# Kernel optimization log

Measured on AMD Instinct MI355X. Metric: run time of the kernel, lower is better.

The kernel has to match this reference:

```python
import jax, jax.numpy as jnp
import numpy as np

NEG_INF = -1e10


def setup_inputs() -> dict:
    key = jax.random.key(0)
    ks = jax.random.split(key, 9)
    B, S, H, E = 64, 4096, 512, 512
    hidden = jax.random.normal(ks[0], (B, H), dtype=jnp.float32)
    encoder_outputs = jax.random.normal(ks[1], (B, S, E), dtype=jnp.float32)
    mask = jax.random.randint(ks[2], (B, S), 0, 2, dtype=jnp.int32)
    s = 1.0 / np.sqrt(H)
    Wq = jax.random.uniform(ks[3], (H, H), jnp.float32, -s, s)
    bq = jax.random.uniform(ks[4], (H,), jnp.float32, -s, s)
    se = 1.0 / np.sqrt(E)
    Wk = jax.random.uniform(ks[5], (E, H), jnp.float32, -se, se)
    bk = jax.random.uniform(ks[6], (H,), jnp.float32, -se, se)
    Wv = jax.random.uniform(ks[7], (H, 1), jnp.float32, -s, s)
    bv = jax.random.uniform(ks[8], (1,), jnp.float32, -s, s)
    return {"hidden": hidden, "encoder_outputs": encoder_outputs, "mask": mask,
            "Wq": Wq, "bq": bq, "Wk": Wk, "bk": bk, "Wv": Wv, "bv": bv}


def reference(hidden, encoder_outputs, mask, Wq, bq, Wk, bk, Wv, bv):
    # query projection: (B, H) -> broadcast over src_len
    q = hidden @ Wq + bq                       # (B, H)
    k = jnp.einsum('bse,eh->bsh', encoder_outputs, Wk) + bk  # (B, S, H)
    energy = jnp.tanh(q[:, None, :] + k)       # (B, S, H)
    scores = jnp.einsum('bsh,h->bs', energy, Wv[:, 0]) + bv[0]  # (B, S)
    scores = jnp.where(mask == 0, NEG_INF, scores)
    attn = jax.nn.softmax(scores, axis=1)      # (B, S)
    context = jnp.einsum('bs,bse->be', attn, encoder_outputs)   # (B, E)
    return context, attn
```

## Files before the change

kernel.cpp:

```cpp
#include <hip/hip_runtime.h>
#include <hip/hip_bf16.h>

#define B_ 64
#define S_ 4096
#define H_ 512
#define E_ 512
#define NEG_INF_ -1e10f

typedef __attribute__((ext_vector_type(8))) short short8;
typedef __attribute__((ext_vector_type(16))) float f32x16;

static __device__ __forceinline__ unsigned short f2bf(float f) {
    union { float f; unsigned u; } v; v.f = f;
    unsigned x = v.u;
    x += 0x7FFFu + ((x >> 16) & 1u);
    return (unsigned short)(x >> 16);
}

static __device__ __forceinline__ unsigned pk2(float lo, float hi) {
    float2 f; f.x = lo; f.y = hi;
    union { __hip_bfloat162 h; unsigned u; } c;
    c.h = __float22bfloat162_rn(f);
    return c.u;
}

static __device__ __forceinline__ void gload_lds16(const void* g, void* l) {
    __builtin_amdgcn_global_load_lds(
        (const __attribute__((address_space(1))) void*)g,
        (__attribute__((address_space(3))) void*)l, 16, 0, 0);
}

#define VMCNT12 do { asm volatile("s_waitcnt vmcnt(12)" ::: "memory"); __builtin_amdgcn_sched_barrier(0); } while (0)
#define VMCNT6  do { asm volatile("s_waitcnt vmcnt(6)"  ::: "memory"); __builtin_amdgcn_sched_barrier(0); } while (0)
#define VMCNT0  do { asm volatile("s_waitcnt vmcnt(0)"  ::: "memory"); __builtin_amdgcn_sched_barrier(0); } while (0)
#define LGKM0   do { asm volatile("s_waitcnt lgkmcnt(0)" ::: "memory"); __builtin_amdgcn_sched_barrier(0); } while (0)

__global__ void prep_wkt(const float* __restrict__ wk, unsigned short* __restrict__ wkt) {
    int idx = blockIdx.x * 256 + threadIdx.x;
    int h = idx >> 9, e = idx & 511;
    wkt[idx] = f2bf(wk[e * H_ + h]);
}

__global__ void prep_qb(const float* __restrict__ hidden, const float* __restrict__ wq,
                        const float* __restrict__ bq, const float* __restrict__ bk,
                        float* __restrict__ qb) {
    __shared__ float hid[H_];
    int b = blockIdx.x, t = threadIdx.x;
    hid[t]       = hidden[b * H_ + t];
    hid[t + 256] = hidden[b * H_ + t + 256];
    __syncthreads();
    for (int hh = t; hh < H_; hh += 256) {
        float s = 0.f;
        for (int e = 0; e < H_; ++e) s += hid[e] * wq[e * H_ + hh];
        qb[b * H_ + hh] = s + bq[hh] + bk[hh];
    }
}

__global__ __launch_bounds__(256, 3) void scores_kernel(
    const float* __restrict__ enc, const unsigned short* __restrict__ wkt,
    const float* __restrict__ qb, const float* __restrict__ wv,
    float* __restrict__ part)
{
    __shared__ char lds[49152];

    int id = blockIdx.x;
    int xcd = id & 7, qq = id >> 3;
    int logical = xcd * 1024 + qq;
    int b  = logical >> 7;
    int r  = logical & 127;
    int st = r >> 2, nt = r & 3;
    int s0 = st * 128;

    const int tid  = threadIdx.x;
    const int lane = tid & 63;
    const int wave = tid >> 6;
    const int wr   = wave >> 1;
    const int wc   = wave & 1;
    const int l31  = lane & 31;
    const int g    = lane >> 5;

    const float* encb = enc + ((size_t)b * S_ + s0) * E_;

    auto loadA = [&](int kc, float4 (&rg)[4]) {
#pragma unroll
        for (int j = 0; j < 2; ++j) {
            int sid = tid * 2 + j;
            int row = sid >> 2, ksl = sid & 3;
            const float* p = encb + (size_t)row * 512 + kc * 32 + ksl * 8;
            rg[j * 2 + 0] = *(const float4*)p;
            rg[j * 2 + 1] = *(const float4*)(p + 4);
        }
    };
    auto writeA = [&](char* buf, const float4 (&rg)[4]) {
#pragma unroll
        for (int j = 0; j < 2; ++j) {
            int sid = tid * 2 + j;
            int row = sid >> 2, ksl = sid & 3;
            int srow = row & 31;
            int sst  = ((row >> 5) * 4 + ksl) ^ (srow & 15);
            union { short8 s; unsigned u[4]; } u;
            u.u[0] = pk2(rg[j * 2].x, rg[j * 2].y);
            u.u[1] = pk2(rg[j * 2].z, rg[j * 2].w);
            u.u[2] = pk2(rg[j * 2 + 1].x, rg[j * 2 + 1].y);
            u.u[3] = pk2(rg[j * 2 + 1].z, rg[j * 2 + 1].w);
            *(short8*)(buf + srow * 256 + sst * 16) = u.s;
        }
    };
    auto stageB = [&](int kc, char* buf) {
#pragma unroll
        for (int p = 0; p < 2; ++p) {
            int gi0 = p * 256 + wave * 64;
            char* db = buf + gi0 * 16;
            int gi = gi0 + lane;
            int sn = gi >> 4, ss = gi & 15;
            int sl = ss ^ (sn & 15);
            int n  = (sl >> 2) * 32 + sn;
            const unsigned short* gp = wkt + (size_t)(nt * 128 + n) * 512 + kc * 32 + (sl & 3) * 8;
            gload_lds16(gp, db);
        }
    };

    f32x16 acc[2][2];
#pragma unroll
    for (int mr = 0; mr < 2; ++mr)
#pragma unroll
        for (int nf = 0; nf < 2; ++nf)
#pragma unroll
            for (int e = 0; e < 16; ++e) acc[mr][nf][e] = 0.f;

    float4 ra[4], rb[4], rc[4];

    stageB(0, lds + 16384);              loadA(0, ra);
    stageB(1, lds + 16384 + 8192);       loadA(1, rb);
    stageB(2, lds + 16384 + 16384);      loadA(2, rc);

    auto iter = [&](int kc, float4 (&rg)[4]) {
        if (kc <= 13) { VMCNT12; } else if (kc == 14) { VMCNT6; } else { VMCNT0; }
        char* Ab = lds + (kc & 1) * 8192;
        writeA(Ab, rg);
        LGKM0;
        __builtin_amdgcn_s_barrier();
        __builtin_amdgcn_sched_barrier(0);
        if (kc < 13) {
            stageB(kc + 3, lds + 16384 + ((kc + 3) & 3) * 8192);
            loadA(kc + 3, rg);
        }
        const char* Bb = lds + 16384 + (kc & 3) * 8192;
#pragma unroll
        for (int ks = 0; ks < 2; ++ks) {
            short8 af[2], bf[2];
#pragma unroll
            for (int mr = 0; mr < 2; ++mr) {
                int sl = (wr * 2 + mr) * 4 + ks * 2 + g;
                af[mr] = *(const short8*)(Ab + l31 * 256 + ((sl ^ (l31 & 15)) << 4));
            }
#pragma unroll
            for (int nf = 0; nf < 2; ++nf) {
                int sl = (wc * 2 + nf) * 4 + ks * 2 + g;
                bf[nf] = *(const short8*)(Bb + l31 * 256 + ((sl ^ (l31 & 15)) << 4));
            }
            acc[0][0] = __builtin_amdgcn_mfma_f32_32x32x16_bf16(af[0], bf[0], acc[0][0], 0, 0, 0);
            acc[0][1] = __builtin_amdgcn_mfma_f32_32x32x16_bf16(af[0], bf[1], acc[0][1], 0, 0, 0);
            acc[1][0] = __builtin_amdgcn_mfma_f32_32x32x16_bf16(af[1], bf[0], acc[1][0], 0, 0, 0);
            acc[1][1] = __builtin_amdgcn_mfma_f32_32x32x16_bf16(af[1], bf[1], acc[1][1], 0, 0, 0);
        }
    };

    for (int t3 = 0; t3 < 5; ++t3) {
        iter(t3 * 3,     ra);
        iter(t3 * 3 + 1, rb);
        iter(t3 * 3 + 2, rc);
    }
    iter(15, ra);

    float p[2][16];
#pragma unroll
    for (int nf = 0; nf < 2; ++nf) {
        int col = nt * 128 + wc * 64 + nf * 32 + l31;
        float qv  = qb[b * H_ + col];
        float wvv = wv[col];
#pragma unroll
        for (int mr = 0; mr < 2; ++mr)
#pragma unroll
            for (int e = 0; e < 16; ++e) {
                float x  = qv + acc[mr][nf][e];
                float ex = __expf(2.f * x);
                float th = 1.f - 2.f / (ex + 1.f);
                float v  = wvv * th;
                p[mr][e] = nf ? (p[mr][e] + v) : v;
            }
    }

    __syncthreads();
    float* ps = (float*)lds;
#pragma unroll
    for (int mr = 0; mr < 2; ++mr)
#pragma unroll
        for (int e = 0; e < 16; ++e) {
            int row = mr * 32 + (e & 3) + 8 * (e >> 2) + 4 * g;
            ps[(wave * 64 + row) * 36 + l31] = p[mr][e];
        }
    __syncthreads();
    float rsum = 0.f;
    {
        const float* myrow = ps + (size_t)(wave * 64 + lane) * 36;
#pragma unroll
        for (int j = 0; j < 8; ++j) {
            float4 v = *(const float4*)(myrow + j * 4);
            rsum += (v.x + v.y) + (v.z + v.w);
        }
    }
    float* pf = (float*)(lds + 37888);
    pf[wave * 64 + lane] = rsum;
    __syncthreads();
    if (tid < 128) {
        int wr2 = tid >> 6, rr = tid & 63;
        float v = pf[(wr2 * 2 + 0) * 64 + rr] + pf[(wr2 * 2 + 1) * 64 + rr];
        int s = s0 + wr2 * 64 + rr;
        part[((size_t)b * S_ + s) * 4 + nt] = v;
    }
}

__global__ void softmax_kernel(const float* __restrict__ part, const int* __restrict__ mask,
                               const float* __restrict__ bvp, float* __restrict__ attn) {
    __shared__ float red[8];
    int b = blockIdx.x, tid = threadIdx.x;
    int wid = tid >> 6, lane = tid & 63;
    float bv0 = bvp[0];
    float vals[8];
    float mx = -3.4e38f;
#pragma unroll
    for (int i = 0; i < 8; ++i) {
        int s = i * 512 + tid;
        float4 v = *(const float4*)(part + ((size_t)b * S_ + s) * 4);
        float sc = (v.x + v.y) + (v.z + v.w) + bv0;
        sc = mask[(size_t)b * S_ + s] ? sc : NEG_INF_;
        vals[i] = sc;
        mx = fmaxf(mx, sc);
    }
#pragma unroll
    for (int off = 1; off < 64; off <<= 1) mx = fmaxf(mx, __shfl_xor(mx, off));
    if (lane == 0) red[wid] = mx;
    __syncthreads();
    mx = red[0];
#pragma unroll
    for (int w = 1; w < 8; ++w) mx = fmaxf(mx, red[w]);
    __syncthreads();
    float sum = 0.f;
#pragma unroll
    for (int i = 0; i < 8; ++i) { vals[i] = __expf(vals[i] - mx); sum += vals[i]; }
#pragma unroll
    for (int off = 1; off < 64; off <<= 1) sum += __shfl_xor(sum, off);
    if (lane == 0) red[wid] = sum;
    __syncthreads();
    sum = red[0] + red[1] + red[2] + red[3] + red[4] + red[5] + red[6] + red[7];
    float inv = 1.f / sum;
#pragma unroll
    for (int i = 0; i < 8; ++i) attn[(size_t)b * S_ + i * 512 + tid] = vals[i] * inv;
}

__global__ void ctx_partial(const float* __restrict__ attn, const float* __restrict__ enc,
                            float* __restrict__ part) {
    __shared__ float a[256];
    int c = blockIdx.x, b = blockIdx.y, t = threadIdx.x;
    a[t] = attn[(size_t)b * S_ + c * 256 + t];
    __syncthreads();
    const float* ep = enc + (size_t)b * S_ * E_ + (size_t)c * 256 * E_ + t * 2;
    float x = 0.f, y = 0.f;
#pragma unroll 4
    for (int s = 0; s < 256; ++s) {
        float2 v = *(const float2*)(ep + (size_t)s * E_);
        x += a[s] * v.x;
        y += a[s] * v.y;
    }
    float* o = part + ((size_t)c * B_ + b) * E_ + t * 2;
    o[0] = x; o[1] = y;
}

__global__ void ctx_reduce(const float* __restrict__ part, float* __restrict__ ctx) {
    int idx = blockIdx.x * 256 + threadIdx.x;
    float s = 0.f;
#pragma unroll
    for (int c = 0; c < 16; ++c) s += part[(size_t)c * (B_ * E_) + idx];
    ctx[idx] = s;
}

extern "C" void kernel_launch(void* const* d_in, const int* in_sizes, int n_in,
                              void* d_out, int out_size, void* d_ws, size_t ws_size,
                              hipStream_t stream) {
    const float* hidden = (const float*)d_in[0];
    const float* enc    = (const float*)d_in[1];
    const int*   mask   = (const int*)d_in[2];
    const float* Wq     = (const float*)d_in[3];
    const float* bq     = (const float*)d_in[4];
    const float* Wk     = (const float*)d_in[5];
    const float* bk     = (const float*)d_in[6];
    const float* Wv     = (const float*)d_in[7];
    const float* bv     = (const float*)d_in[8];

    float* out  = (float*)d_out;
    char*  ws   = (char*)d_ws;
    float*          qbuf   = (float*)ws;
    unsigned short* wkt    = (unsigned short*)(ws + 131072);
    float*          pscore = (float*)(ws + 655360);
    float*          cpart  = (float*)(ws + 655360);

    float* ctx  = out;
    float* attn = out + B_ * E_;

    prep_wkt<<<1024, 256, 0, stream>>>(Wk, wkt);
    prep_qb<<<64, 256, 0, stream>>>(hidden, Wq, bq, bk, qbuf);
    scores_kernel<<<8192, 256, 0, stream>>>(enc, wkt, qbuf, Wv, pscore);
    softmax_kernel<<<64, 512, 0, stream>>>(pscore, mask, bv, attn);
    ctx_partial<<<dim3(16, 64), 256, 0, stream>>>(attn, enc, cpart);
    ctx_reduce<<<128, 256, 0, stream>>>(cpart, ctx);
}
```

Baseline: 434.4 us.

## Feed A fragments directly from registers, dropping the LDS staging of encoder tile

Each wave now owns 32 full rows of the 128-row tile and loads its encoder rows straight into registers in MFMA operand layout. It converts them to bf16 in place instead of writing them to LDS and reading them back. This removes the A-tile LDS writes, the lgkmcnt wait and the A fragment reads, and shrinks shared memory from 48KB to 32KB, which may allow more resident blocks. In exchange each wave reads all four B fragments per k-step (more LDS B traffic), and the global load pattern changes to 32-byte strided row chunks, which may coalesce less well.

```diff
diff --git a/kernel.cpp b/kernel.cpp
--- a/kernel.cpp
+++ b/kernel.cpp
@@ -33,7 +33,6 @@
 #define VMCNT12 do { asm volatile("s_waitcnt vmcnt(12)" ::: "memory"); __builtin_amdgcn_sched_barrier(0); } while (0)
 #define VMCNT6  do { asm volatile("s_waitcnt vmcnt(6)"  ::: "memory"); __builtin_amdgcn_sched_barrier(0); } while (0)
 #define VMCNT0  do { asm volatile("s_waitcnt vmcnt(0)"  ::: "memory"); __builtin_amdgcn_sched_barrier(0); } while (0)
-#define LGKM0   do { asm volatile("s_waitcnt lgkmcnt(0)" ::: "memory"); __builtin_amdgcn_sched_barrier(0); } while (0)
 
 __global__ void prep_wkt(const float* __restrict__ wk, unsigned short* __restrict__ wkt) {
     int idx = blockIdx.x * 256 + threadIdx.x;
@@ -61,7 +60,7 @@
     const float* __restrict__ qb, const float* __restrict__ wv,
     float* __restrict__ part)
 {
-    __shared__ char lds[49152];
+    __shared__ char lds[32768];
 
     int id = blockIdx.x;
     int xcd = id & 7, qq = id >> 3;
@@ -74,37 +73,17 @@
     const int tid  = threadIdx.x;
     const int lane = tid & 63;
     const int wave = tid >> 6;
-    const int wr   = wave >> 1;
-    const int wc   = wave & 1;
     const int l31  = lane & 31;
     const int g    = lane >> 5;
 
-    const float* encb = enc + ((size_t)b * S_ + s0) * E_;
+    const float* aRow = enc + ((size_t)b * S_ + s0 + wave * 32 + l31) * E_ + g * 8;
 
     auto loadA = [&](int kc, float4 (&rg)[4]) {
-#pragma unroll
-        for (int j = 0; j < 2; ++j) {
-            int sid = tid * 2 + j;
-            int row = sid >> 2, ksl = sid & 3;
-            const float* p = encb + (size_t)row * 512 + kc * 32 + ksl * 8;
-            rg[j * 2 + 0] = *(const float4*)p;
-            rg[j * 2 + 1] = *(const float4*)(p + 4);
-        }
-    };
-    auto writeA = [&](char* buf, const float4 (&rg)[4]) {
-#pragma unroll
-        for (int j = 0; j < 2; ++j) {
-            int sid = tid * 2 + j;
-            int row = sid >> 2, ksl = sid & 3;
-            int srow = row & 31;
-            int sst  = ((row >> 5) * 4 + ksl) ^ (srow & 15);
-            union { short8 s; unsigned u[4]; } u;
-            u.u[0] = pk2(rg[j * 2].x, rg[j * 2].y);
-            u.u[1] = pk2(rg[j * 2].z, rg[j * 2].w);
-            u.u[2] = pk2(rg[j * 2 + 1].x, rg[j * 2 + 1].y);
-            u.u[3] = pk2(rg[j * 2 + 1].z, rg[j * 2 + 1].w);
-            *(short8*)(buf + srow * 256 + sst * 16) = u.s;
-        }
+        const float* p = aRow + kc * 32;
+        rg[0] = *(const float4*)(p);
+        rg[1] = *(const float4*)(p + 4);
+        rg[2] = *(const float4*)(p + 16);
+        rg[3] = *(const float4*)(p + 20);
     };
     auto stageB = [&](int kc, char* buf) {
 #pragma unroll
@@ -120,49 +99,44 @@
         }
     };
 
-    f32x16 acc[2][2];
-#pragma unroll
-    for (int mr = 0; mr < 2; ++mr)
-#pragma unroll
-        for (int nf = 0; nf < 2; ++nf)
-#pragma unroll
-            for (int e = 0; e < 16; ++e) acc[mr][nf][e] = 0.f;
+    f32x16 acc[4];
+#pragma unroll
+    for (int nf = 0; nf < 4; ++nf)
+#pragma unroll
+        for (int e = 0; e < 16; ++e) acc[nf][e] = 0.f;
 
     float4 ra[4], rb[4], rc[4];
 
-    stageB(0, lds + 16384);              loadA(0, ra);
-    stageB(1, lds + 16384 + 8192);       loadA(1, rb);
-    stageB(2, lds + 16384 + 16384);      loadA(2, rc);
+    stageB(0, lds);                  loadA(0, ra);
+    stageB(1, lds + 8192);           loadA(1, rb);
+    stageB(2, lds + 16384);          loadA(2, rc);
 
     auto iter = [&](int kc, float4 (&rg)[4]) {
         if (kc <= 13) { VMCNT12; } else if (kc == 14) { VMCNT6; } else { VMCNT0; }
-        char* Ab = lds + (kc & 1) * 8192;
-        writeA(Ab, rg);
-        LGKM0;
+        short8 af[2];
+        {
+            union { short8 s; unsigned u[4]; } u0, u1;
+            u0.u[0] = pk2(rg[0].x, rg[0].y); u0.u[1] = pk2(rg[0].z, rg[0].w);
+            u0.u[2] = pk2(rg[1].x, rg[1].y); u0.u[3] = pk2(rg[1].z, rg[1].w);
+            u1.u[0] = pk2(rg[2].x, rg[2].y); u1.u[1] = pk2(rg[2].z, rg[2].w);
+            u1.u[2] = pk2(rg[3].x, rg[3].y); u1.u[3] = pk2(rg[3].z, rg[3].w);
+            af[0] = u0.s; af[1] = u1.s;
+        }
         __builtin_amdgcn_s_barrier();
         __builtin_amdgcn_sched_barrier(0);
         if (kc < 13) {
-            stageB(kc + 3, lds + 16384 + ((kc + 3) & 3) * 8192);
+            stageB(kc + 3, lds + ((kc + 3) & 3) * 8192);
             loadA(kc + 3, rg);
         }
-        const char* Bb = lds + 16384 + (kc & 3) * 8192;
+        const char* Bb = lds + (kc & 3) * 8192;
 #pragma unroll
         for (int ks = 0; ks < 2; ++ks) {
-            short8 af[2], bf[2];
-#pragma unroll
-            for (int mr = 0; mr < 2; ++mr) {
-                int sl = (wr * 2 + mr) * 4 + ks * 2 + g;
-                af[mr] = *(const short8*)(Ab + l31 * 256 + ((sl ^ (l31 & 15)) << 4));
+#pragma unroll
+            for (int nf = 0; nf < 4; ++nf) {
+                int sl = nf * 4 + ks * 2 + g;
+                short8 bf = *(const short8*)(Bb + l31 * 256 + ((sl ^ (l31 & 15)) << 4));
+                acc[nf] = __builtin_amdgcn_mfma_f32_32x32x16_bf16(af[ks], bf, acc[nf], 0, 0, 0);
             }
-#pragma unroll
-            for (int nf = 0; nf < 2; ++nf) {
-                int sl = (wc * 2 + nf) * 4 + ks * 2 + g;
-                bf[nf] = *(const short8*)(Bb + l31 * 256 + ((sl ^ (l31 & 15)) << 4));
-            }
-            acc[0][0] = __builtin_amdgcn_mfma_f32_32x32x16_bf16(af[0], bf[0], acc[0][0], 0, 0, 0);
-            acc[0][1] = __builtin_amdgcn_mfma_f32_32x32x16_bf16(af[0], bf[1], acc[0][1], 0, 0, 0);
-            acc[1][0] = __builtin_amdgcn_mfma_f32_32x32x16_bf16(af[1], bf[0], acc[1][0], 0, 0, 0);
-            acc[1][1] = __builtin_amdgcn_mfma_f32_32x32x16_bf16(af[1], bf[1], acc[1][1], 0, 0, 0);
         }
     };
 
@@ -173,51 +147,48 @@
     }
     iter(15, ra);
 
-    float p[2][16];
-#pragma unroll
-    for (int nf = 0; nf < 2; ++nf) {
-        int col = nt * 128 + wc * 64 + nf * 32 + l31;
+    float p[16];
+#pragma unroll
+    for (int nf = 0; nf < 4; ++nf) {
+        int col = nt * 128 + nf * 32 + l31;
         float qv  = qb[b * H_ + col];
         float wvv = wv[col];
 #pragma unroll
-        for (int mr = 0; mr < 2; ++mr)
-#pragma unroll
-            for (int e = 0; e < 16; ++e) {
-                float x  = qv + acc[mr][nf][e];
-                float ex = __expf(2.f * x);
-                float th = 1.f - 2.f / (ex + 1.f);
-                float v  = wvv * th;
-                p[mr][e] = nf ? (p[mr][e] + v) : v;
-            }
+        for (int e = 0; e < 16; ++e) {
+            float x  = qv + acc[nf][e];
+            float ex = __expf(2.f * x);
+            float th = 1.f - 2.f / (ex + 1.f);
+            float v  = wvv * th;
+            p[e] = nf ? (p[e] + v) : v;
+        }
     }
 
     __syncthreads();
     float* ps = (float*)lds;
 #pragma unroll
-    for (int mr = 0; mr < 2; ++mr)
-#pragma unroll
-        for (int e = 0; e < 16; ++e) {
-            int row = mr * 32 + (e & 3) + 8 * (e >> 2) + 4 * g;
-            ps[(wave * 64 + row) * 36 + l31] = p[mr][e];
-        }
-    __syncthreads();
-    float rsum = 0.f;
+    for (int e = 0; e < 16; ++e) {
+        int row = wave * 32 + (e & 3) + 8 * (e >> 2) + 4 * g;
+        ps[row * 36 + l31] = p[e];
+    }
+    __syncthreads();
     {
-        const float* myrow = ps + (size_t)(wave * 64 + lane) * 36;
-#pragma unroll
-        for (int j = 0; j < 8; ++j) {
+        int rr   = tid & 127;
+        int half = tid >> 7;
+        const float* myrow = ps + rr * 36 + half * 16;
+        float rsum = 0.f;
+#pragma unroll
+        for (int j = 0; j < 4; ++j) {
             float4 v = *(const float4*)(myrow + j * 4);
             rsum += (v.x + v.y) + (v.z + v.w);
         }
-    }
-    float* pf = (float*)(lds + 37888);
-    pf[wave * 64 + lane] = rsum;
-    __syncthreads();
-    if (tid < 128) {
-        int wr2 = tid >> 6, rr = tid & 63;
-        float v = pf[(wr2 * 2 + 0) * 64 + rr] + pf[(wr2 * 2 + 1) * 64 + rr];
-        int s = s0 + wr2 * 64 + rr;
-        part[((size_t)b * S_ + s) * 4 + nt] = v;
+        float* pf = (float*)(lds + 18432);
+        pf[half * 128 + rr] = rsum;
+        __syncthreads();
+        if (tid < 128) {
+            float v = pf[tid] + pf[128 + tid];
+            int s = s0 + tid;
+            part[((size_t)b * S_ + s) * 4 + nt] = v;
+        }
     }
 }
 
```

Result: slower. 580.9 us (+33.7%).
